# Optimization experiments

Hardware: AMD Instinct MI355X
Metric: run time of the kernel (lower is better)

Reference implementation:

```python
import jax, jax.numpy as jnp
import numpy as np

B = 1024
INPUT_SIZE = 2048
OUTPUT_SIZE = 2048
E = 131072  # number of sparse connections


def setup_inputs() -> dict:
    key = jax.random.key(0)
    k1, k2, k3, k4 = jax.random.split(key, 4)
    x = jax.random.normal(k1, (B, INPUT_SIZE), dtype=jnp.float32)
    weights = jax.random.normal(k2, (E,), dtype=jnp.float32)
    in_idx = jax.random.randint(k3, (E,), 0, INPUT_SIZE, dtype=jnp.int64)
    out_idx = jax.random.randint(k4, (E,), 0, OUTPUT_SIZE, dtype=jnp.int64)
    return {"x": x, "weights": weights, "in_idx": in_idx, "out_idx": out_idx}


def reference(x, weights, in_idx, out_idx):
    # Original: for (i, o), w in connections: output[:, o] += w * x[:, i]
    # Vectorized as a single gather-multiply-scatter (duplicates sum):
    contrib = x[:, in_idx] * weights[None, :]  # [B, E]
    out = jnp.zeros((x.shape[0], OUTPUT_SIZE), dtype=x.dtype)
    out = out.at[:, out_idx].add(contrib)  # scatter-add along output dim
    return out
```

## Files before the change

### kernel.cpp

```cpp
#include <hip/hip_runtime.h>
#include <hip/hip_bf16.h>

#define BATCH  1024
#define IN_SZ  2048
#define OUT_SZ 2048
#define E_N    131072

#define K_MAX  128
#define NT     256
#define R8     8
#define CG     (OUT_SZ / NT)
#define RG     (BATCH / R8)

__device__ __forceinline__ unsigned int bf16_rne(float f) {
    unsigned int u = __float_as_uint(f);
    return (u + 0x7FFFu + ((u >> 16) & 1u)) >> 16;
}

__global__ void fill_kernel(const int* __restrict__ iidx, const int* __restrict__ oidx,
                            const float* __restrict__ w,
                            int* __restrict__ cursor, unsigned int* __restrict__ ell) {
    const int e = blockIdx.x * 256 + threadIdx.x;
    const int o = oidx[e];
    const int i = iidx[e];
    const unsigned int wb = bf16_rne(w[e]) << 16;
    const int pos = atomicAdd(&cursor[o], 1);
    if (pos < K_MAX)
        ell[(size_t)pos * OUT_SZ + o] = wb | (unsigned int)(i << 4);
}

__global__ __launch_bounds__(NT) void spmm_kernel(const float* __restrict__ x,
                                                  const unsigned int* __restrict__ ell,
                                                  const int* __restrict__ cursor,
                                                  float* __restrict__ out) {
    __shared__ __align__(16) unsigned short xsT[IN_SZ * R8];
    const int cg  = blockIdx.x;
    const int r0  = blockIdx.y * R8;
    const int tid = threadIdx.x;

    const float* xb = x + (size_t)r0 * IN_SZ;
    #pragma unroll
    for (int it = 0; it < IN_SZ / NT; ++it) {
        const int c = it * NT + tid;
        unsigned int p[4];
        #pragma unroll
        for (int j = 0; j < 4; ++j) {
            const float lo = xb[(size_t)(2 * j) * IN_SZ + c];
            const float hi = xb[(size_t)(2 * j + 1) * IN_SZ + c];
            p[j] = (bf16_rne(hi) << 16) | bf16_rne(lo);
        }
        *(uint4*)&xsT[c * R8] = make_uint4(p[0], p[1], p[2], p[3]);
    }
    __syncthreads();

    const int c = cg * NT + tid;
    int cnt = cursor[c];
    #pragma unroll
    for (int off = 32; off > 0; off >>= 1) {
        const int other = __shfl_xor(cnt, off);
        cnt = cnt > other ? cnt : other;
    }
    cnt = cnt < K_MAX ? cnt : K_MAX;

    float acc[R8];
    #pragma unroll
    for (int r = 0; r < R8; r++) acc[r] = 0.f;

    const unsigned int* ep = ell + c;
    #pragma unroll 4
    for (int k = 0; k < cnt; ++k) {
        const unsigned int e = ep[(size_t)k * OUT_SZ];
        const float wv = __uint_as_float(e & 0xFFFF0000u);
        const uint4 xv = *(const uint4*)((const char*)xsT + (e & 0xFFFFu));
        acc[0] = fmaf(wv, __uint_as_float(xv.x << 16),          acc[0]);
        acc[1] = fmaf(wv, __uint_as_float(xv.x & 0xFFFF0000u),  acc[1]);
        acc[2] = fmaf(wv, __uint_as_float(xv.y << 16),          acc[2]);
        acc[3] = fmaf(wv, __uint_as_float(xv.y & 0xFFFF0000u),  acc[3]);
        acc[4] = fmaf(wv, __uint_as_float(xv.z << 16),          acc[4]);
        acc[5] = fmaf(wv, __uint_as_float(xv.z & 0xFFFF0000u),  acc[5]);
        acc[6] = fmaf(wv, __uint_as_float(xv.w << 16),          acc[6]);
        acc[7] = fmaf(wv, __uint_as_float(xv.w & 0xFFFF0000u),  acc[7]);
    }

    float* op = out + (size_t)r0 * OUT_SZ + c;
    #pragma unroll
    for (int r = 0; r < R8; r++) op[(size_t)r * OUT_SZ] = acc[r];
}

__global__ __launch_bounds__(NT) void sparse_row_kernel(
    const float* __restrict__ x, const float* __restrict__ w,
    const int* __restrict__ iidx, const int* __restrict__ oidx,
    float* __restrict__ out) {
    __shared__ float xs[IN_SZ];
    __shared__ float acc[OUT_SZ];
    const int b = blockIdx.x, tid = threadIdx.x;
    const float4* xrow = (const float4*)(x + (size_t)b * IN_SZ);
    float4* xs4 = (float4*)xs;
    for (int t = tid; t < IN_SZ / 4; t += NT) xs4[t] = xrow[t];
    float4* acc4 = (float4*)acc;
    const float4 z = make_float4(0.f, 0.f, 0.f, 0.f);
    for (int t = tid; t < OUT_SZ / 4; t += NT) acc4[t] = z;
    __syncthreads();
    for (int e = tid; e < E_N; e += NT)
        atomicAdd(&acc[oidx[e]], w[e] * xs[iidx[e]]);
    __syncthreads();
    float4* orow = (float4*)(out + (size_t)b * OUT_SZ);
    for (int t = tid; t < OUT_SZ / 4; t += NT) orow[t] = acc4[t];
}

extern "C" void kernel_launch(void* const* d_in, const int* in_sizes, int n_in,
                              void* d_out, int out_size, void* d_ws, size_t ws_size,
                              hipStream_t stream) {
    const float* x    = (const float*)d_in[0];
    const float* wts  = (const float*)d_in[1];
    const int*   iidx = (const int*)d_in[2];
    const int*   oidx = (const int*)d_in[3];
    float* out = (float*)d_out;
    (void)in_sizes; (void)n_in; (void)out_size;

    const size_t need = (size_t)OUT_SZ * sizeof(int)
                      + (size_t)K_MAX * OUT_SZ * sizeof(unsigned int);
    if (ws_size < need) {
        sparse_row_kernel<<<BATCH, NT, 0, stream>>>(x, wts, iidx, oidx, out);
        return;
    }

    int* cursor = (int*)d_ws;
    unsigned int* ell = (unsigned int*)(cursor + OUT_SZ);

    hipMemsetAsync(d_ws, 0, need, stream);
    fill_kernel<<<E_N / 256, 256, 0, stream>>>(iidx, oidx, wts, cursor, ell);
    dim3 grid(CG, RG);
    spmm_kernel<<<grid, NT, 0, stream>>>(x, ell, cursor, out);
}
```

Measured before the change: 109.3 us.

## Fuse memset, ELL fill and SpMM into one cooperative grid-synced kernel

```diff
diff --git a/kernel.cpp b/kernel.cpp
--- a/kernel.cpp
+++ b/kernel.cpp
@@ -1,20 +1,101 @@
 #include <hip/hip_runtime.h>
 #include <hip/hip_bf16.h>
+#include <hip/hip_cooperative_groups.h>
+
+namespace cg = cooperative_groups;
 
 #define BATCH  1024
 #define IN_SZ  2048
 #define OUT_SZ 2048
 #define E_N    131072
 
-#define K_MAX  128
 #define NT     256
 #define R8     8
-#define CG     (OUT_SZ / NT)
-#define RG     (BATCH / R8)
+#define CGN    8
+#define RGN    (BATCH / R8)
+#define NBLK   (CGN * RGN)
+#define NSEG   2
+#define SEG_D  64
+#define K_MAX  (NSEG * SEG_D)
 
 __device__ __forceinline__ unsigned int bf16_rne(float f) {
     unsigned int u = __float_as_uint(f);
     return (u + 0x7FFFu + ((u >> 16) & 1u)) >> 16;
+}
+
+__global__ __launch_bounds__(NT) void fused_kernel(
+    const float* __restrict__ x, const float* __restrict__ w,
+    const int* __restrict__ iidx, const int* __restrict__ oidx,
+    int* __restrict__ cursor,
+    unsigned int* __restrict__ ell,
+    float* __restrict__ out) {
+    __shared__ __align__(16) unsigned short xsT[IN_SZ * R8];
+    const int bid = blockIdx.x;
+    const int tid = threadIdx.x;
+
+    if (bid < (NSEG * OUT_SZ) / NT) cursor[bid * NT + tid] = 0;
+
+    const int cgid = bid & (CGN - 1);
+    const int r0   = (bid >> 3) * R8;
+    const float* xb = x + (size_t)r0 * IN_SZ;
+    #pragma unroll
+    for (int it = 0; it < IN_SZ / NT; ++it) {
+        const int c = it * NT + tid;
+        unsigned int p[4];
+        #pragma unroll
+        for (int j = 0; j < 4; ++j) {
+            const float lo = xb[(size_t)(2 * j) * IN_SZ + c];
+            const float hi = xb[(size_t)(2 * j + 1) * IN_SZ + c];
+            p[j] = (bf16_rne(hi) << 16) | bf16_rne(lo);
+        }
+        *(uint4*)&xsT[c * R8] = make_uint4(p[0], p[1], p[2], p[3]);
+    }
+
+    cg::this_grid().sync();
+
+    if (tid < E_N / NBLK) {
+        const int e = bid * (E_N / NBLK) + tid;
+        const int o = oidx[e];
+        const int i = iidx[e];
+        const unsigned int wb = bf16_rne(w[e]) << 16;
+        const int s = e >> 16;
+        const int pos = atomicAdd(&cursor[s * OUT_SZ + o], 1);
+        if (pos < SEG_D)
+            ell[(size_t)(s * SEG_D + pos) * OUT_SZ + o] = wb | (unsigned int)(i << 4);
+    }
+    __threadfence();
+
+    cg::this_grid().sync();
+
+    const int c = cgid * NT + tid;
+    float acc[R8];
+    #pragma unroll
+    for (int r = 0; r < R8; r++) acc[r] = 0.f;
+
+    #pragma unroll
+    for (int s = 0; s < NSEG; ++s) {
+        int cnt = cursor[s * OUT_SZ + c];
+        cnt = cnt < SEG_D ? cnt : SEG_D;
+        const unsigned int* ep = ell + (size_t)(s * SEG_D) * OUT_SZ + c;
+        #pragma unroll 4
+        for (int k = 0; k < cnt; ++k) {
+            const unsigned int e = ep[(size_t)k * OUT_SZ];
+            const float wv = __uint_as_float(e & 0xFFFF0000u);
+            const uint4 xv = *(const uint4*)((const char*)xsT + (e & 0xFFFFu));
+            acc[0] = fmaf(wv, __uint_as_float(xv.x << 16),         acc[0]);
+            acc[1] = fmaf(wv, __uint_as_float(xv.x & 0xFFFF0000u), acc[1]);
+            acc[2] = fmaf(wv, __uint_as_float(xv.y << 16),         acc[2]);
+            acc[3] = fmaf(wv, __uint_as_float(xv.y & 0xFFFF0000u), acc[3]);
+            acc[4] = fmaf(wv, __uint_as_float(xv.z << 16),         acc[4]);
+            acc[5] = fmaf(wv, __uint_as_float(xv.z & 0xFFFF0000u), acc[5]);
+            acc[6] = fmaf(wv, __uint_as_float(xv.w << 16),         acc[6]);
+            acc[7] = fmaf(wv, __uint_as_float(xv.w & 0xFFFF0000u), acc[7]);
+        }
+    }
+
+    float* op = out + (size_t)r0 * OUT_SZ + c;
+    #pragma unroll
+    for (int r = 0; r < R8; r++) op[(size_t)r * OUT_SZ] = acc[r];
 }
 
 __global__ void fill_kernel(const int* __restrict__ iidx, const int* __restrict__ oidx,
@@ -24,9 +105,10 @@
     const int o = oidx[e];
     const int i = iidx[e];
     const unsigned int wb = bf16_rne(w[e]) << 16;
-    const int pos = atomicAdd(&cursor[o], 1);
-    if (pos < K_MAX)
-        ell[(size_t)pos * OUT_SZ + o] = wb | (unsigned int)(i << 4);
+    const int s = e >> 16;
+    const int pos = atomicAdd(&cursor[s * OUT_SZ + o], 1);
+    if (pos < SEG_D)
+        ell[(size_t)(s * SEG_D + pos) * OUT_SZ + o] = wb | (unsigned int)(i << 4);
 }
 
 __global__ __launch_bounds__(NT) void spmm_kernel(const float* __restrict__ x,
@@ -34,10 +116,9 @@
                                                   const int* __restrict__ cursor,
                                                   float* __restrict__ out) {
     __shared__ __align__(16) unsigned short xsT[IN_SZ * R8];
-    const int cg  = blockIdx.x;
-    const int r0  = blockIdx.y * R8;
-    const int tid = threadIdx.x;
-
+    const int cgid = blockIdx.x;
+    const int r0   = blockIdx.y * R8;
+    const int tid  = threadIdx.x;
     const float* xb = x + (size_t)r0 * IN_SZ;
     #pragma unroll
     for (int it = 0; it < IN_SZ / NT; ++it) {
@@ -53,59 +134,33 @@
     }
     __syncthreads();
 
-    const int c = cg * NT + tid;
-    int cnt = cursor[c];
-    #pragma unroll
-    for (int off = 32; off > 0; off >>= 1) {
-        const int other = __shfl_xor(cnt, off);
-        cnt = cnt > other ? cnt : other;
-    }
-    cnt = cnt < K_MAX ? cnt : K_MAX;
-
+    const int c = cgid * NT + tid;
     float acc[R8];
     #pragma unroll
     for (int r = 0; r < R8; r++) acc[r] = 0.f;
-
-    const unsigned int* ep = ell + c;
-    #pragma unroll 4
-    for (int k = 0; k < cnt; ++k) {
-        const unsigned int e = ep[(size_t)k * OUT_SZ];
-        const float wv = __uint_as_float(e & 0xFFFF0000u);
-        const uint4 xv = *(const uint4*)((const char*)xsT + (e & 0xFFFFu));
-        acc[0] = fmaf(wv, __uint_as_float(xv.x << 16),          acc[0]);
-        acc[1] = fmaf(wv, __uint_as_float(xv.x & 0xFFFF0000u),  acc[1]);
-        acc[2] = fmaf(wv, __uint_as_float(xv.y << 16),          acc[2]);
-        acc[3] = fmaf(wv, __uint_as_float(xv.y & 0xFFFF0000u),  acc[3]);
-        acc[4] = fmaf(wv, __uint_as_float(xv.z << 16),          acc[4]);
-        acc[5] = fmaf(wv, __uint_as_float(xv.z & 0xFFFF0000u),  acc[5]);
-        acc[6] = fmaf(wv, __uint_as_float(xv.w << 16),          acc[6]);
-        acc[7] = fmaf(wv, __uint_as_float(xv.w & 0xFFFF0000u),  acc[7]);
+    #pragma unroll
+    for (int s = 0; s < NSEG; ++s) {
+        int cnt = cursor[s * OUT_SZ + c];
+        cnt = cnt < SEG_D ? cnt : SEG_D;
+        const unsigned int* ep = ell + (size_t)(s * SEG_D) * OUT_SZ + c;
+        #pragma unroll 4
+        for (int k = 0; k < cnt; ++k) {
+            const unsigned int e = ep[(size_t)k * OUT_SZ];
+            const float wv = __uint_as_float(e & 0xFFFF0000u);
+            const uint4 xv = *(const uint4*)((const char*)xsT + (e & 0xFFFFu));
+            acc[0] = fmaf(wv, __uint_as_float(xv.x << 16),         acc[0]);
+            acc[1] = fmaf(wv, __uint_as_float(xv.x & 0xFFFF0000u), acc[1]);
+            acc[2] = fmaf(wv, __uint_as_float(xv.y << 16),         acc[2]);
+            acc[3] = fmaf(wv, __uint_as_float(xv.y & 0xFFFF0000u), acc[3]);
+            acc[4] = fmaf(wv, __uint_as_float(xv.z << 16),         acc[4]);
+            acc[5] = fmaf(wv, __uint_as_float(xv.z & 0xFFFF0000u), acc[5]);
+            acc[6] = fmaf(wv, __uint_as_float(xv.w << 16),         acc[6]);
+            acc[7] = fmaf(wv, __uint_as_float(xv.w & 0xFFFF0000u), acc[7]);
+        }
     }
-
     float* op = out + (size_t)r0 * OUT_SZ + c;
     #pragma unroll
     for (int r = 0; r < R8; r++) op[(size_t)r * OUT_SZ] = acc[r];
-}
-
-__global__ __launch_bounds__(NT) void sparse_row_kernel(
-    const float* __restrict__ x, const float* __restrict__ w,
-    const int* __restrict__ iidx, const int* __restrict__ oidx,
-    float* __restrict__ out) {
-    __shared__ float xs[IN_SZ];
-    __shared__ float acc[OUT_SZ];
-    const int b = blockIdx.x, tid = threadIdx.x;
-    const float4* xrow = (const float4*)(x + (size_t)b * IN_SZ);
-    float4* xs4 = (float4*)xs;
-    for (int t = tid; t < IN_SZ / 4; t += NT) xs4[t] = xrow[t];
-    float4* acc4 = (float4*)acc;
-    const float4 z = make_float4(0.f, 0.f, 0.f, 0.f);
-    for (int t = tid; t < OUT_SZ / 4; t += NT) acc4[t] = z;
-    __syncthreads();
-    for (int e = tid; e < E_N; e += NT)
-        atomicAdd(&acc[oidx[e]], w[e] * xs[iidx[e]]);
-    __syncthreads();
-    float4* orow = (float4*)(out + (size_t)b * OUT_SZ);
-    for (int t = tid; t < OUT_SZ / 4; t += NT) orow[t] = acc4[t];
 }
 
 extern "C" void kernel_launch(void* const* d_in, const int* in_sizes, int n_in,
@@ -118,18 +173,18 @@
     float* out = (float*)d_out;
     (void)in_sizes; (void)n_in; (void)out_size;
 
-    const size_t need = (size_t)OUT_SZ * sizeof(int)
-                      + (size_t)K_MAX * OUT_SZ * sizeof(unsigned int);
-    if (ws_size < need) {
-        sparse_row_kernel<<<BATCH, NT, 0, stream>>>(x, wts, iidx, oidx, out);
-        return;
+    int* cursor = (int*)d_ws;
+    unsigned int* ell = (unsigned int*)(cursor + NSEG * OUT_SZ);
+
+    void* args[] = { (void*)&x, (void*)&wts, (void*)&iidx, (void*)&oidx,
+                     (void*)&cursor, (void*)&ell, (void*)&out };
+    hipError_t err = hipLaunchCooperativeKernel((const void*)fused_kernel,
+                                                dim3(NBLK), dim3(NT),
+                                                args, 0, stream);
+    if (err != hipSuccess) {
+        hipMemsetAsync(cursor, 0, (size_t)NSEG * OUT_SZ * sizeof(int), stream);
+        fill_kernel<<<E_N / 256, 256, 0, stream>>>(iidx, oidx, wts, cursor, ell);
+        dim3 grid(CGN, RGN);
+        spmm_kernel<<<grid, NT, 0, stream>>>(x, ell, cursor, out);
     }
-
-    int* cursor = (int*)d_ws;
-    unsigned int* ell = (unsigned int*)(cursor + OUT_SZ);
-
-    hipMemsetAsync(d_ws, 0, need, stream);
-    fill_kernel<<<E_N / 256, 256, 0, stream>>>(iidx, oidx, wts, cursor, ell);
-    dim3 grid(CG, RG);
-    spmm_kernel<<<grid, NT, 0, stream>>>(x, ell, cursor, out);
 }
```

Result: slower. 407.7 us (+273.0%).

## Split ELL build into two segments with padded per-segment atomic counters

Applied to the files above, without the earlier changes.

```diff
diff --git a/kernel.cpp b/kernel.cpp
--- a/kernel.cpp
+++ b/kernel.cpp
@@ -6,11 +6,14 @@
 #define OUT_SZ 2048
 #define E_N    131072
 
-#define K_MAX  128
 #define NT     256
 #define R8     8
-#define CG     (OUT_SZ / NT)
-#define RG     (BATCH / R8)
+#define CGN    8
+#define RGN    (BATCH / R8)
+#define NSEG   2
+#define SEG_D  64
+#define K_MAX  (NSEG * SEG_D)
+#define CPAD   16
 
 __device__ __forceinline__ unsigned int bf16_rne(float f) {
     unsigned int u = __float_as_uint(f);
@@ -24,9 +27,10 @@
     const int o = oidx[e];
     const int i = iidx[e];
     const unsigned int wb = bf16_rne(w[e]) << 16;
-    const int pos = atomicAdd(&cursor[o], 1);
-    if (pos < K_MAX)
-        ell[(size_t)pos * OUT_SZ + o] = wb | (unsigned int)(i << 4);
+    const int s = e >> 16;
+    const int pos = atomicAdd(&cursor[(s * OUT_SZ + o) * CPAD], 1);
+    if (pos < SEG_D)
+        ell[(size_t)(s * SEG_D + pos) * OUT_SZ + o] = wb | (unsigned int)(i << 4);
 }
 
 __global__ __launch_bounds__(NT) void spmm_kernel(const float* __restrict__ x,
@@ -34,9 +38,9 @@
                                                   const int* __restrict__ cursor,
                                                   float* __restrict__ out) {
     __shared__ __align__(16) unsigned short xsT[IN_SZ * R8];
-    const int cg  = blockIdx.x;
-    const int r0  = blockIdx.y * R8;
-    const int tid = threadIdx.x;
+    const int cgid = blockIdx.x;
+    const int r0   = blockIdx.y * R8;
+    const int tid  = threadIdx.x;
 
     const float* xb = x + (size_t)r0 * IN_SZ;
     #pragma unroll
@@ -53,33 +57,30 @@
     }
     __syncthreads();
 
-    const int c = cg * NT + tid;
-    int cnt = cursor[c];
-    #pragma unroll
-    for (int off = 32; off > 0; off >>= 1) {
-        const int other = __shfl_xor(cnt, off);
-        cnt = cnt > other ? cnt : other;
-    }
-    cnt = cnt < K_MAX ? cnt : K_MAX;
-
+    const int c = cgid * NT + tid;
     float acc[R8];
     #pragma unroll
     for (int r = 0; r < R8; r++) acc[r] = 0.f;
 
-    const unsigned int* ep = ell + c;
-    #pragma unroll 4
-    for (int k = 0; k < cnt; ++k) {
-        const unsigned int e = ep[(size_t)k * OUT_SZ];
-        const float wv = __uint_as_float(e & 0xFFFF0000u);
-        const uint4 xv = *(const uint4*)((const char*)xsT + (e & 0xFFFFu));
-        acc[0] = fmaf(wv, __uint_as_float(xv.x << 16),          acc[0]);
-        acc[1] = fmaf(wv, __uint_as_float(xv.x & 0xFFFF0000u),  acc[1]);
-        acc[2] = fmaf(wv, __uint_as_float(xv.y << 16),          acc[2]);
-        acc[3] = fmaf(wv, __uint_as_float(xv.y & 0xFFFF0000u),  acc[3]);
-        acc[4] = fmaf(wv, __uint_as_float(xv.z << 16),          acc[4]);
-        acc[5] = fmaf(wv, __uint_as_float(xv.z & 0xFFFF0000u),  acc[5]);
-        acc[6] = fmaf(wv, __uint_as_float(xv.w << 16),          acc[6]);
-        acc[7] = fmaf(wv, __uint_as_float(xv.w & 0xFFFF0000u),  acc[7]);
+    #pragma unroll
+    for (int s = 0; s < NSEG; ++s) {
+        int cnt = cursor[(s * OUT_SZ + c) * CPAD];
+        cnt = cnt < SEG_D ? cnt : SEG_D;
+        const unsigned int* ep = ell + (size_t)(s * SEG_D) * OUT_SZ + c;
+        #pragma unroll 4
+        for (int k = 0; k < cnt; ++k) {
+            const unsigned int e = ep[(size_t)k * OUT_SZ];
+            const float wv = __uint_as_float(e & 0xFFFF0000u);
+            const uint4 xv = *(const uint4*)((const char*)xsT + (e & 0xFFFFu));
+            acc[0] = fmaf(wv, __uint_as_float(xv.x << 16),         acc[0]);
+            acc[1] = fmaf(wv, __uint_as_float(xv.x & 0xFFFF0000u), acc[1]);
+            acc[2] = fmaf(wv, __uint_as_float(xv.y << 16),         acc[2]);
+            acc[3] = fmaf(wv, __uint_as_float(xv.y & 0xFFFF0000u), acc[3]);
+            acc[4] = fmaf(wv, __uint_as_float(xv.z << 16),         acc[4]);
+            acc[5] = fmaf(wv, __uint_as_float(xv.z & 0xFFFF0000u), acc[5]);
+            acc[6] = fmaf(wv, __uint_as_float(xv.w << 16),         acc[6]);
+            acc[7] = fmaf(wv, __uint_as_float(xv.w & 0xFFFF0000u), acc[7]);
+        }
     }
 
     float* op = out + (size_t)r0 * OUT_SZ + c;
@@ -118,18 +119,18 @@
     float* out = (float*)d_out;
     (void)in_sizes; (void)n_in; (void)out_size;
 
-    const size_t need = (size_t)OUT_SZ * sizeof(int)
-                      + (size_t)K_MAX * OUT_SZ * sizeof(unsigned int);
+    const size_t cursor_bytes = (size_t)NSEG * OUT_SZ * CPAD * sizeof(int);
+    const size_t need = cursor_bytes + (size_t)K_MAX * OUT_SZ * sizeof(unsigned int);
     if (ws_size < need) {
         sparse_row_kernel<<<BATCH, NT, 0, stream>>>(x, wts, iidx, oidx, out);
         return;
     }
 
     int* cursor = (int*)d_ws;
-    unsigned int* ell = (unsigned int*)(cursor + OUT_SZ);
+    unsigned int* ell = (unsigned int*)((char*)d_ws + cursor_bytes);
 
-    hipMemsetAsync(d_ws, 0, need, stream);
+    hipMemsetAsync(cursor, 0, cursor_bytes, stream);
     fill_kernel<<<E_N / 256, 256, 0, stream>>>(iidx, oidx, wts, cursor, ell);
-    dim3 grid(CG, RG);
+    dim3 grid(CGN, RGN);
     spmm_kernel<<<grid, NT, 0, stream>>>(x, ell, cursor, out);
 }
```

New measurement: 99.03 us. 1.1x faster.
